# Performance work log

Measured on AMD Instinct MI355X. Metric: run time of the kernel, lower is better.

Reference implementation:

```python
import jax, jax.numpy as jnp
import numpy as np

NUM_EXPERTS = 64
NOISE_STD = 1.0
CAPACITY = 32  # top-C items per expert (experts-choice routing)
D_MODEL = 512
NUM_GROUPS = 8
GROUP_SIZE = 2048


def _top_items_per_expert_dispatcher(gates):
    """Experts-choice dispatcher for one group.

    gates: (S, E) softmax gate values.
    Returns:
      dispatch: (E, C, S) one-hot selection of the top-C items per expert.
      combine:  (S, E, C) gate value if item s is expert e's c-th pick, else 0.
    """
    s = gates.shape[0]
    # Each expert picks its top-C items by gate value.
    _, top_idx = jax.lax.top_k(gates.T, CAPACITY)          # (E, C)
    dispatch = jax.nn.one_hot(top_idx, s, dtype=gates.dtype)  # (E, C, S)
    combine = jnp.einsum('se,ecs->sec', gates, dispatch)      # (S, E, C)
    return dispatch, combine


def setup_inputs() -> dict:
    key = jax.random.key(0)
    k1, k2 = jax.random.split(key)
    inputs = jax.random.normal(k1, (NUM_GROUPS, GROUP_SIZE, D_MODEL), dtype=jnp.float32)
    # Dense(num_experts, use_bias=False) kernel, lecun-normal-ish scale.
    W = jax.random.normal(k2, (D_MODEL, NUM_EXPERTS), dtype=jnp.float32) * (D_MODEL ** -0.5)
    return {"inputs": inputs, "W": W}


def reference(inputs, W):
    # Gating projection: (G, S, D) x (D, E) -> (G, S, E)
    logits = jnp.einsum('gsd,de->gse', inputs, W)
    # Noisy gating: noise_std scaled by 1/num_experts (as in the module).
    noise_scale = NOISE_STD / NUM_EXPERTS
    noise = noise_scale * jax.random.normal(jax.random.key(42), logits.shape, dtype=logits.dtype)
    gates = jax.nn.softmax(logits + noise, axis=-1)  # (G, S, E)
    # vmap the per-group top-items-per-expert dispatcher over groups.
    dispatch, combine = jax.vmap(_top_items_per_expert_dispatcher)(gates)
    return combine, dispatch
```

## Files before the change

### kernel.cpp

```cpp
#include <hip/hip_runtime.h>
#include <math.h>
#include <stdint.h>

#define NG 8
#define GS 2048
#define DM 512
#define NE 64
#define CAP 32
#define NROWS (NG * GS)
#define COMBINE_ELEMS (33554432ull)

#define GATE_BLOCKS 512
#define XST 516
#define TBS 21

typedef float f32x4 __attribute__((ext_vector_type(4)));
typedef double f64x2 __attribute__((ext_vector_type(2)));
typedef double f64x4 __attribute__((ext_vector_type(4)));
typedef unsigned long long u64;

__device__ __forceinline__ void threefry2x32(uint32_t k0, uint32_t k1,
                                             uint32_t x0, uint32_t x1,
                                             uint32_t& o0, uint32_t& o1) {
  uint32_t ks[3] = {k0, k1, k0 ^ k1 ^ 0x1BD11BDAu};
  x0 += ks[0];
  x1 += ks[1];
  const uint32_t rot[2][4] = {{13u, 15u, 26u, 6u}, {17u, 29u, 16u, 24u}};
#pragma unroll
  for (int i = 0; i < 5; ++i) {
#pragma unroll
    for (int j = 0; j < 4; ++j) {
      uint32_t r = rot[i & 1][j];
      x0 += x1;
      x1 = (x1 << r) | (x1 >> (32u - r));
      x1 ^= x0;
    }
    x0 += ks[(i + 1) % 3];
    x1 += ks[(i + 2) % 3] + (uint32_t)(i + 1);
  }
  o0 = x0;
  o1 = x1;
}

__device__ __forceinline__ float erfinv_xla(float x) {
  float w = -log1pf(-x * x);
  float p;
  if (w < 5.0f) {
    w = w - 2.5f;
    p = 2.81022636e-08f;
    p = __fmaf_rn(p, w, 3.43273939e-07f);
    p = __fmaf_rn(p, w, -3.5233877e-06f);
    p = __fmaf_rn(p, w, -4.39150654e-06f);
    p = __fmaf_rn(p, w, 0.00021858087f);
    p = __fmaf_rn(p, w, -0.00125372503f);
    p = __fmaf_rn(p, w, -0.00417768164f);
    p = __fmaf_rn(p, w, 0.246640727f);
    p = __fmaf_rn(p, w, 1.50140941f);
  } else {
    w = sqrtf(w) - 3.0f;
    p = -0.000200214257f;
    p = __fmaf_rn(p, w, 0.000100950558f);
    p = __fmaf_rn(p, w, 0.00134934322f);
    p = __fmaf_rn(p, w, -0.00367342844f);
    p = __fmaf_rn(p, w, 0.00573950773f);
    p = __fmaf_rn(p, w, -0.0076224613f);
    p = __fmaf_rn(p, w, 0.00943887047f);
    p = __fmaf_rn(p, w, 1.00167406f);
    p = __fmaf_rn(p, w, 2.83297682f);
  }
  return p * x;
}

__device__ __forceinline__ float jax_normal(uint32_t idx) {
  uint32_t o0, o1;
  threefry2x32(0u, 42u, 0u, idx, o0, o1);
  uint32_t bits = o0 ^ o1;
  float f = __uint_as_float((bits >> 9) | 0x3f800000u) - 1.0f;
  const float lo = __uint_as_float(0xBF7FFFFFu);
  float v = fmaxf(lo, f * 2.0f + lo);
  return __uint_as_float(0x3FB504F3u) * erfinv_xla(v);
}

__global__ __launch_bounds__(256) void wprep_kernel(
    const float* __restrict__ Wt, double* __restrict__ Wd) {
  const int i = blockIdx.x * 256 + threadIdx.x;
  const int t = i & 3, i15 = (i >> 2) & 15, row = i >> 6;
  Wd[i] = (double)Wt[row * NE + t * 16 + i15];
}

__global__ __launch_bounds__(256) void gate_kernel(
    const float* __restrict__ x,
    const double* __restrict__ Wd,
    float* __restrict__ gatesT) {
  __shared__ float xs[32 * XST];
  const int gid = blockIdx.x;
  const int tid = threadIdx.x;
  const int l = tid & 63;
  const int w4 = tid >> 6;
  const int wr = w4 & 1;
  const int kh = w4 >> 1;
  const int row0b = gid * 32;
  const int row0 = row0b + wr * 16;

  const int i15 = l & 15;
  const int k4 = l >> 4;

  f64x4 dr = {0., 0., 0., 0.};
  dr = __builtin_amdgcn_mfma_f64_16x16x4f64((double)i15, 0.25, dr, 0, 0, 0);
  int perm[4];
#pragma unroll
  for (int r = 0; r < 4; ++r) perm[r] = ((int)(dr[r] + 0.5)) & 15;

#pragma unroll 8
  for (int i = tid; i < 4096; i += 256) {
    const int r = i >> 7, c = (i & 127) << 2;
    *(f32x4*)&xs[r * XST + c] =
        *(const f32x4*)&x[(size_t)(row0b + r) * DM + c];
  }
  __syncthreads();

  f64x4 acc[4] = {{0., 0., 0., 0.}, {0., 0., 0., 0.},
                  {0., 0., 0., 0.}, {0., 0., 0., 0.}};
  const float* xrow = &xs[(wr * 16 + i15) * XST + k4];
  const double* wl = Wd + k4 * 64 + i15 * 4;
  const int kk0 = kh * 64;
  f64x2 b01 = *(const f64x2*)(wl + (size_t)kk0 * 256 + 0);
  f64x2 b23 = *(const f64x2*)(wl + (size_t)kk0 * 256 + 2);
#pragma unroll 4
  for (int kk = kk0; kk < kk0 + 64; ++kk) {
    const int nk = (kk + 1) & 127;
    const f64x2 nb01 = *(const f64x2*)(wl + (size_t)nk * 256 + 0);
    const f64x2 nb23 = *(const f64x2*)(wl + (size_t)nk * 256 + 2);
    const double a = (double)xrow[kk * 4];
    acc[0] = __builtin_amdgcn_mfma_f64_16x16x4f64(a, b01[0], acc[0], 0, 0, 0);
    acc[1] = __builtin_amdgcn_mfma_f64_16x16x4f64(a, b01[1], acc[1], 0, 0, 0);
    acc[2] = __builtin_amdgcn_mfma_f64_16x16x4f64(a, b23[0], acc[2], 0, 0, 0);
    acc[3] = __builtin_amdgcn_mfma_f64_16x16x4f64(a, b23[1], acc[3], 0, 0, 0);
    b01 = nb01;
    b23 = nb23;
  }
  __syncthreads();

  double* pd = (double*)&xs[4096];
  if (kh == 1) {
    double* dst = pd + ((size_t)(wr * 64 + l)) * 16;
#pragma unroll
    for (int t = 0; t < 4; ++t)
#pragma unroll
      for (int r = 0; r < 4; ++r) dst[t * 4 + r] = acc[t][r];
  }
  __syncthreads();
  if (kh == 1) return;

  {
    const double* src = pd + ((size_t)(wr * 64 + l)) * 16;
#pragma unroll
    for (int t = 0; t < 4; ++t)
#pragma unroll
      for (int r = 0; r < 4; ++r) acc[t][r] += src[t * 4 + r];
  }

  float gatef[4][4];
#pragma unroll
  for (int r = 0; r < 4; ++r) {
    const int row = row0 + perm[r];
    double v[4];
    double m = -1.0e300;
#pragma unroll
    for (int t = 0; t < 4; ++t) {
      const float logit = (float)acc[t][r];
      const float noised =
          logit + 0.015625f * jax_normal((uint32_t)(row * NE + 16 * t + i15));
      v[t] = (double)noised;
      m = fmax(m, v[t]);
    }
#pragma unroll
    for (int off = 1; off < 16; off <<= 1) m = fmax(m, __shfl_xor(m, off, 64));
    double s = 0.0;
#pragma unroll
    for (int t = 0; t < 4; ++t) {
      v[t] = exp(v[t] - m);
      s += v[t];
    }
#pragma unroll
    for (int off = 1; off < 16; off <<= 1) s += __shfl_xor(s, off, 64);
#pragma unroll
    for (int t = 0; t < 4; ++t) gatef[t][r] = (float)(v[t] / s);
  }

  float* tb = xs + wr * (NE * TBS);
#pragma unroll
  for (int t = 0; t < 4; ++t)
#pragma unroll
    for (int r = 0; r < 4; ++r)
      tb[(16 * t + i15) * TBS + perm[r]] = gatef[t][r];

  const int g = row0 >> 11;
  const int s0 = row0 & (GS - 1);
  float* drow = gatesT + ((size_t)(g * NE + l)) * GS + s0;
#pragma unroll
  for (int c = 0; c < 4; ++c) {
    f32x4 o;
#pragma unroll
    for (int i = 0; i < 4; ++i) o[i] = tb[l * TBS + 4 * c + i];
    *(f32x4*)&drow[4 * c] = o;
  }
}

__global__ __launch_bounds__(256) void topwrite_kernel(
    const float* __restrict__ gatesT,
    float* __restrict__ out) {
  __shared__ u64 keys[CAP];
  __shared__ int sel_s[CAP];
  __shared__ float sel_v[CAP];
  __shared__ unsigned char c_of_s[GS];
  const int ge = blockIdx.x;
  const int g = ge >> 6, e = ge & 63;
  const int tid = threadIdx.x;
  const int lane = tid & 63, w = tid >> 6;

  ((u64*)c_of_s)[tid] = ~0ull;

  if (w == 0) {
    const float* base = gatesT + (size_t)ge * GS;
    u64 K[32];
#pragma unroll
    for (int k = 0; k < 8; ++k) {
      const f32x4 t = *(const f32x4*)(base + k * 256 + lane * 4);
#pragma unroll
      for (int i = 0; i < 4; ++i) {
        const int s = k * 256 + lane * 4 + i;
        K[k * 4 + i] = ((u64)__float_as_uint(t[i]) << 32) | (u64)(2047 - s);
      }
    }
#pragma unroll
    for (int k = 2; k <= 32; k <<= 1) {
#pragma unroll
      for (int d = k >> 1; d > 0; d >>= 1) {
#pragma unroll
        for (int j = 0; j < 32; ++j) {
          const int ixj = j ^ d;
          if (ixj > j) {
            const bool asc = ((j & k) == 0);
            const u64 a = K[j], b = K[ixj];
            const bool sw = asc ? (a > b) : (a < b);
            K[j] = sw ? b : a;
            K[ixj] = sw ? a : b;
          }
        }
      }
    }
#pragma unroll
    for (int m = 1; m < 64; m <<= 1) {
      u64 tmp[32];
#pragma unroll
      for (int j = 0; j < 32; ++j) tmp[j] = __shfl_xor(K[31 - j], m, 64);
#pragma unroll
      for (int j = 0; j < 32; ++j) K[j] = (K[j] > tmp[j]) ? K[j] : tmp[j];
#pragma unroll
      for (int d = 16; d > 0; d >>= 1) {
#pragma unroll
        for (int j = 0; j < 32; ++j) {
          if ((j & d) == 0) {
            const u64 a = K[j], b = K[j | d];
            const bool sw = (a > b);
            K[j] = sw ? b : a;
            K[j | d] = sw ? a : b;
          }
        }
      }
    }
#pragma unroll
    for (int c = 0; c < CAP; ++c) {
      if (lane == c) keys[c] = K[31 - c];
    }
  }
  __syncthreads();

  if (tid < CAP) {
    const u64 key = keys[tid];
    sel_s[tid] = 2047 - (int)(key & 0x7FFull);
    sel_v[tid] = __uint_as_float((uint32_t)(key >> 32));
  }
  __syncthreads();
  if (tid < CAP) c_of_s[sel_s[tid]] = (unsigned char)tid;
  __syncthreads();

  float* drow_base = out + COMBINE_ELEMS + (size_t)ge * CAP * GS;
#pragma unroll
  for (int rr = 0; rr < 8; ++rr) {
    const int c = 8 * w + rr;
    const int sc = sel_s[c];
    float* rowp = drow_base + (size_t)c * GS;
#pragma unroll
    for (int j = 0; j < 8; ++j) {
      const int pos = j * 256 + lane * 4;
      f32x4 v;
      v[0] = (sc == pos + 0) ? 1.0f : 0.0f;
      v[1] = (sc == pos + 1) ? 1.0f : 0.0f;
      v[2] = (sc == pos + 2) ? 1.0f : 0.0f;
      v[3] = (sc == pos + 3) ? 1.0f : 0.0f;
      *(f32x4*)&rowp[pos] = v;
    }
  }

  const int pos = (lane & 7) * 4;
  for (int it = 0; it < 64; ++it) {
    const int s = 512 * w + 8 * it + (lane >> 3);
    const int c = c_of_s[s];
    const float val = (c != 255) ? sel_v[c & 31] : 0.0f;
    const int d = c - pos;
    f32x4 v;
    v[0] = (d == 0) ? val : 0.0f;
    v[1] = (d == 1) ? val : 0.0f;
    v[2] = (d == 2) ? val : 0.0f;
    v[3] = (d == 3) ? val : 0.0f;
    *(f32x4*)&out[(((size_t)(g * GS + s)) * NE + e) * CAP + pos] = v;
  }
}

extern "C" void kernel_launch(void* const* d_in, const int* in_sizes, int n_in,
                              void* d_out, int out_size, void* d_ws,
                              size_t ws_size, hipStream_t stream) {
  (void)in_sizes; (void)n_in; (void)ws_size; (void)out_size;
  const float* x = (const float*)d_in[0];
  const float* Wt = (const float*)d_in[1];
  float* out = (float*)d_out;
  float* gatesT = (float*)d_ws;
  double* Wd = (double*)((char*)d_ws + ((size_t)NROWS * NE * 4));

  wprep_kernel<<<128, 256, 0, stream>>>(Wt, Wd);
  gate_kernel<<<GATE_BLOCKS, 256, 0, stream>>>(x, Wd, gatesT);
  topwrite_kernel<<<NG * NE, 256, 0, stream>>>(gatesT, out);
}
```

Measured before the change: 115.5 us.

## Double-buffer gating input chunks in LDS to overlap loads with MFMA

The gate kernel no longer stages the whole 32x512 input tile into shared memory before computing. It now streams the K dimension in 64-column chunks through two LDS buffers, prefetching the next chunk into registers while MFMAs run on the current one. This cuts LDS footprint, which can raise occupancy, and hides global load latency behind compute. The cost is a barrier per chunk and loss of the previous software prefetch of W rows.

```diff
diff --git a/kernel.cpp b/kernel.cpp
--- a/kernel.cpp
+++ b/kernel.cpp
@@ -11,7 +11,8 @@
 #define COMBINE_ELEMS (33554432ull)
 
 #define GATE_BLOCKS 512
-#define XST 516
+#define XSTc 68
+#define CHW (32 * XSTc)
 #define TBS 21
 
 typedef float f32x4 __attribute__((ext_vector_type(4)));
@@ -92,7 +93,8 @@
     const float* __restrict__ x,
     const double* __restrict__ Wd,
     float* __restrict__ gatesT) {
-  __shared__ float xs[32 * XST];
+  __shared__ float xs[2 * CHW];
+  __shared__ double pd[128 * 16];
   const int gid = blockIdx.x;
   const int tid = threadIdx.x;
   const int l = tid & 63;
@@ -111,37 +113,56 @@
 #pragma unroll
   for (int r = 0; r < 4; ++r) perm[r] = ((int)(dr[r] + 0.5)) & 15;
 
-#pragma unroll 8
-  for (int i = tid; i < 4096; i += 256) {
-    const int r = i >> 7, c = (i & 127) << 2;
-    *(f32x4*)&xs[r * XST + c] =
-        *(const f32x4*)&x[(size_t)(row0b + r) * DM + c];
+  const int sr0 = tid >> 4, sc0 = (tid & 15) << 2;
+  const int sr1 = (tid + 256) >> 4, sc1 = ((tid + 256) & 15) << 2;
+  const float* xg0 = x + (size_t)(row0b + sr0) * DM + sc0;
+  const float* xg1 = x + (size_t)(row0b + sr1) * DM + sc1;
+  float* xl0 = xs + sr0 * XSTc + sc0;
+  float* xl1 = xs + sr1 * XSTc + sc1;
+
+  {
+    const f32x4 a0 = *(const f32x4*)xg0;
+    const f32x4 a1 = *(const f32x4*)xg1;
+    *(f32x4*)xl0 = a0;
+    *(f32x4*)xl1 = a1;
   }
   __syncthreads();
 
   f64x4 acc[4] = {{0., 0., 0., 0.}, {0., 0., 0., 0.},
                   {0., 0., 0., 0.}, {0., 0., 0., 0.}};
-  const float* xrow = &xs[(wr * 16 + i15) * XST + k4];
-  const double* wl = Wd + k4 * 64 + i15 * 4;
-  const int kk0 = kh * 64;
-  f64x2 b01 = *(const f64x2*)(wl + (size_t)kk0 * 256 + 0);
-  f64x2 b23 = *(const f64x2*)(wl + (size_t)kk0 * 256 + 2);
-#pragma unroll 4
-  for (int kk = kk0; kk < kk0 + 64; ++kk) {
-    const int nk = (kk + 1) & 127;
-    const f64x2 nb01 = *(const f64x2*)(wl + (size_t)nk * 256 + 0);
-    const f64x2 nb23 = *(const f64x2*)(wl + (size_t)nk * 256 + 2);
-    const double a = (double)xrow[kk * 4];
-    acc[0] = __builtin_amdgcn_mfma_f64_16x16x4f64(a, b01[0], acc[0], 0, 0, 0);
-    acc[1] = __builtin_amdgcn_mfma_f64_16x16x4f64(a, b01[1], acc[1], 0, 0, 0);
-    acc[2] = __builtin_amdgcn_mfma_f64_16x16x4f64(a, b23[0], acc[2], 0, 0, 0);
-    acc[3] = __builtin_amdgcn_mfma_f64_16x16x4f64(a, b23[1], acc[3], 0, 0, 0);
-    b01 = nb01;
-    b23 = nb23;
-  }
-  __syncthreads();
-
-  double* pd = (double*)&xs[4096];
+  const int abase = (wr * 16 + i15) * XSTc + k4;
+  const int kl0 = kh * 8;
+  for (int ck = 0; ck < 8; ++ck) {
+    const int cur = ck & 1;
+    f32x4 a0, a1;
+    const bool more = (ck < 7);
+    if (more) {
+      a0 = *(const f32x4*)(xg0 + (ck + 1) * 64);
+      a1 = *(const f32x4*)(xg1 + (ck + 1) * 64);
+    }
+    const float* ar = xs + cur * CHW + abase;
+#pragma unroll
+    for (int kkl = 0; kkl < 8; ++kkl) {
+      const int kloc = kl0 + kkl;
+      const double a = (double)ar[kloc * 4];
+      const int kk = ck * 16 + kloc;
+      const double* wrow = Wd + ((size_t)((kk << 2) + k4)) * 64 + i15 * 4;
+      const f64x2 b01 = *(const f64x2*)(wrow + 0);
+      const f64x2 b23 = *(const f64x2*)(wrow + 2);
+      acc[0] = __builtin_amdgcn_mfma_f64_16x16x4f64(a, b01[0], acc[0], 0, 0, 0);
+      acc[1] = __builtin_amdgcn_mfma_f64_16x16x4f64(a, b01[1], acc[1], 0, 0, 0);
+      acc[2] = __builtin_amdgcn_mfma_f64_16x16x4f64(a, b23[0], acc[2], 0, 0, 0);
+      acc[3] = __builtin_amdgcn_mfma_f64_16x16x4f64(a, b23[1], acc[3], 0, 0, 0);
+    }
+    if (more) {
+      float* d0 = xs + (cur ^ 1) * CHW + sr0 * XSTc + sc0;
+      float* d1 = xs + (cur ^ 1) * CHW + sr1 * XSTc + sc1;
+      *(f32x4*)d0 = a0;
+      *(f32x4*)d1 = a1;
+    }
+    __syncthreads();
+  }
+
   if (kh == 1) {
     double* dst = pd + ((size_t)(wr * 64 + l)) * 16;
 #pragma unroll
```

Result: faster. 105.1 us (median of 2 runs) (-8.9%).
